# Optimization experiments

Measured on AMD Instinct MI355X. Metric: run time of the kernel, lower is better.

Reference implementation:

```python
import jax, jax.numpy as jnp
import numpy as np

B, S, D = 2, 2048, 1024
H = 16
HD = D // H  # 64
EPS = 1e-6
ROPE_BASE = 10000.0


def _rms_norm(x, w, eps=EPS):
    # torch nn.RMSNorm over last dim
    var = jnp.mean(jnp.square(x), axis=-1, keepdims=True)
    return x * jax.lax.rsqrt(var + eps) * w


def _rope_tables(seq_len, head_dim, base=ROPE_BASE):
    inv_freq = 1.0 / (base ** (jnp.arange(0, head_dim, 2, dtype=jnp.float32) / head_dim))
    t = jnp.arange(seq_len, dtype=jnp.float32)
    freqs = t[:, None] * inv_freq[None, :]            # [S, HD/2]
    emb = jnp.concatenate([freqs, freqs], axis=-1)    # [S, HD]
    return jnp.cos(emb), jnp.sin(emb)


def _rotate_half(x):
    x1, x2 = jnp.split(x, 2, axis=-1)
    return jnp.concatenate([-x2, x1], axis=-1)


def _apply_rope(x, cos, sin):
    # x: [B, H, S, HD]; cos/sin: [S, HD]
    return x * cos[None, None] + _rotate_half(x) * sin[None, None]


def setup_inputs() -> dict:
    key = jax.random.key(0)
    ks = jax.random.split(key, 8)
    scale = 1.0 / np.sqrt(D)
    return {
        "x": jax.random.normal(ks[0], (B, S, D), dtype=jnp.float32),
        "wq": jax.random.normal(ks[1], (D, D), dtype=jnp.float32) * scale,
        "wk": jax.random.normal(ks[2], (D, D), dtype=jnp.float32) * scale,
        "wv": jax.random.normal(ks[3], (D, D), dtype=jnp.float32) * scale,
        "wo": jax.random.normal(ks[4], (D, D), dtype=jnp.float32) * scale,
        "q_norm_w": jnp.ones((HD,), dtype=jnp.float32),
        "k_norm_w": jnp.ones((HD,), dtype=jnp.float32),
        "sink_logit": jnp.zeros((H,), dtype=jnp.float32),
    }


def reference(x, wq, wk, wv, wo, q_norm_w, k_norm_w, sink_logit):
    b, s, _ = x.shape
    # QKV projections (nn.Linear, no bias): y = x @ W^T
    q = jnp.einsum("bsd,od->bso", x, wq).reshape(b, s, H, HD)
    k = jnp.einsum("bsd,od->bso", x, wk).reshape(b, s, H, HD)
    v = jnp.einsum("bsd,od->bso", x, wv).reshape(b, s, H, HD)
    # QK RMSNorm (per head_dim)
    q = _rms_norm(q, q_norm_w)
    k = _rms_norm(k, k_norm_w)
    # [B, H, S, HD]
    q = q.transpose(0, 2, 1, 3)
    k = k.transpose(0, 2, 1, 3)
    v = v.transpose(0, 2, 1, 3)
    # full-head RoPE
    cos, sin = _rope_tables(s, HD)
    q = _apply_rope(q, cos, sin)
    k = _apply_rope(k, cos, sin)
    # manual attention with causal mask and sink softmax
    scale = HD ** -0.5
    scores = jnp.einsum("bhqd,bhkd->bhqk", q, k) * scale  # [B,H,S,S]
    causal = jnp.tril(jnp.ones((s, s), dtype=bool))
    scores = jnp.where(causal[None, None], scores, -jnp.inf)
    # sink-augmented softmax in fp32: append per-head sink logit, softmax, drop sink column
    sink = jnp.broadcast_to(sink_logit.astype(jnp.float32)[None, :, None, None], (b, H, s, 1))
    aug = jnp.concatenate([scores.astype(jnp.float32), sink], axis=-1)
    weights = jax.nn.softmax(aug, axis=-1)[..., :s].astype(scores.dtype)
    out = jnp.einsum("bhqk,bhkd->bhqd", weights, v)
    out = out.transpose(0, 2, 1, 3).reshape(b, s, D)
    return jnp.einsum("bsd,od->bso", out, wo)
```

## Files before the change

### kernel.cpp

```cpp
#include <hip/hip_runtime.h>

#define Bb 2
#define Ss 2048
#define Dd 1024
#define Hh 16
#define HDd 64
#define BS (Bb * Ss)

typedef __attribute__((ext_vector_type(8))) __bf16 bf16x8;
typedef __attribute__((ext_vector_type(8))) unsigned short u16x8;
typedef __attribute__((ext_vector_type(4))) float f32x4;

__device__ __forceinline__ unsigned short f2bf(float f) {
  union { float f; unsigned u; } v; v.f = f;
  unsigned r = v.u + 0x7fffu + ((v.u >> 16) & 1u);
  return (unsigned short)(r >> 16);
}
__device__ __forceinline__ unsigned short f2bf_fast(float f) {
  union { float f; unsigned u; } v; v.f = f;
  return (unsigned short)((v.u + 0x8000u) >> 16);
}

__device__ __forceinline__ void gl_lds16(const void* g, void* l) {
  __builtin_amdgcn_global_load_lds(
      (const __attribute__((address_space(1))) void*)g,
      (__attribute__((address_space(3))) void*)l, 16, 0, 0);
}

__global__ __launch_bounds__(256) void cast_all(
    const float4* __restrict__ x, const float4* __restrict__ wq,
    const float4* __restrict__ wk, const float4* __restrict__ wv,
    const float4* __restrict__ wo, ushort4* __restrict__ xb,
    ushort4* __restrict__ wqkvb, ushort4* __restrict__ wob,
    float* __restrict__ ct, float* __restrict__ st) {
  int i = blockIdx.x * 256 + threadIdx.x;
  const int NX4 = BS * Dd / 4;
  const int NW4 = Dd * Dd / 4;
  const float4* src;
  ushort4* dst;
  int idx;
  if (i < NX4) { src = x; dst = xb; idx = i; }
  else if ((i -= NX4) < NW4) { src = wq; dst = wqkvb; idx = i; }
  else if ((i -= NW4) < NW4) { src = wk; dst = wqkvb + NW4; idx = i; }
  else if ((i -= NW4) < NW4) { src = wv; dst = wqkvb + 2 * NW4; idx = i; }
  else if ((i -= NW4) < NW4) { src = wo; dst = wob; idx = i; }
  else if ((i -= NW4) < Ss * 32) {
    int s = i >> 5, jj = i & 31;
    float freq = __powf(10000.0f, -(float)jj * (1.0f / 32.0f));
    float cs, sn;
    sincosf((float)s * freq, &sn, &cs);
    ct[i] = cs; st[i] = sn;
    return;
  } else return;
  float4 v = src[idx];
  ushort4 o;
  o.x = f2bf(v.x); o.y = f2bf(v.y); o.z = f2bf(v.z); o.w = f2bf(v.w);
  dst[idx] = o;
}

__global__ __launch_bounds__(256, 3) void gemm_qkv(
    const unsigned short* __restrict__ A, const unsigned short* __restrict__ Bw,
    const float* __restrict__ qw, const float* __restrict__ kw,
    const float* __restrict__ ct, const float* __restrict__ st,
    unsigned short* __restrict__ Qb, unsigned short* __restrict__ Kb,
    unsigned short* __restrict__ Vt) {
  __shared__ __align__(16) unsigned short As[128 * 32];
  __shared__ __align__(16) unsigned short Bs[128 * 32];
  const int K = Dd, tid = threadIdx.x;
  const int lane = tid & 63;
  const int quad = lane >> 4;
  const int l16 = lane & 15;
  const int wave = tid >> 6;
  const int wm = (wave >> 1) * 64;
  const int wn = (wave & 1) * 64;
  const int tile_m = blockIdx.y * 128;
  const int tile_n = blockIdx.x * 128;

  const int off0 = tid * 16;
  const int off1 = 4096 + tid * 16;
  const int r0 = tid >> 2, r1 = r0 + 64;
  const int sch = (((tid & 3) ^ ((tid >> 3) & 3)) << 3);
  const int xg = ((quad ^ ((l16 >> 1) & 3)) << 3);

  const unsigned short* Ag0 = A + (size_t)(tile_m + r0) * K + sch;
  const unsigned short* Ag1 = A + (size_t)(tile_m + r1) * K + sch;
  const unsigned short* Bg0 = Bw + (size_t)(tile_n + r0) * K + sch;
  const unsigned short* Bg1 = Bw + (size_t)(tile_n + r1) * K + sch;

  f32x4 zero = {0.f, 0.f, 0.f, 0.f};
  f32x4 acc[4][4];
#pragma unroll
  for (int mi = 0; mi < 4; ++mi)
#pragma unroll
    for (int ni = 0; ni < 4; ++ni) acc[mi][ni] = zero;

  for (int k0 = 0; k0 < K; k0 += 32) {
    gl_lds16(Ag0 + k0, (char*)As + off0);
    gl_lds16(Ag1 + k0, (char*)As + off1);
    gl_lds16(Bg0 + k0, (char*)Bs + off0);
    gl_lds16(Bg1 + k0, (char*)Bs + off1);
    __syncthreads();
    bf16x8 af[4], bfv[4];
#pragma unroll
    for (int mi = 0; mi < 4; ++mi)
      af[mi] = *(const bf16x8*)&As[(wm + mi * 16 + l16) * 32 + xg];
#pragma unroll
    for (int ni = 0; ni < 4; ++ni)
      bfv[ni] = *(const bf16x8*)&Bs[(wn + ni * 16 + l16) * 32 + xg];
#pragma unroll
    for (int mi = 0; mi < 4; ++mi)
#pragma unroll
      for (int ni = 0; ni < 4; ++ni)
        acc[mi][ni] = __builtin_amdgcn_mfma_f32_16x16x32_bf16(
            af[mi], bfv[ni], acc[mi][ni], 0, 0, 0);
    __syncthreads();
  }

  const int type = blockIdx.x >> 3;
  const int h = (((blockIdx.x & 7) << 7) + wn) >> 6;
  const int bb = tile_m >> 11;
  const size_t bh = (size_t)bb * Hh + h;

  if (type == 2) {
#pragma unroll
    for (int mi = 0; mi < 4; ++mi) {
      int s0 = (tile_m + wm + mi * 16 + quad * 4) & (Ss - 1);
#pragma unroll
      for (int ni = 0; ni < 4; ++ni) {
        int d = ni * 16 + l16;
        ushort4 pv;
        pv.x = f2bf(acc[mi][ni][0]);
        pv.y = f2bf(acc[mi][ni][1]);
        pv.z = f2bf(acc[mi][ni][2]);
        pv.w = f2bf(acc[mi][ni][3]);
        *(ushort4*)&Vt[(bh * HDd + d) * Ss + s0] = pv;
      }
    }
  } else {
    const float* wnp = type ? kw : qw;
    unsigned short* Ob = type ? Kb : Qb;
    const float fscale = type ? 1.0f : 0.125f * 1.44269504f;
    float w0[4];
#pragma unroll
    for (int ni = 0; ni < 4; ++ni) w0[ni] = wnp[ni * 16 + l16];
#pragma unroll
    for (int mi = 0; mi < 4; ++mi) {
#pragma unroll
      for (int r = 0; r < 4; ++r) {
        int s = (tile_m + wm + mi * 16 + quad * 4 + r) & (Ss - 1);
        float ss2 = 0.f;
#pragma unroll
        for (int ni = 0; ni < 4; ++ni) ss2 += acc[mi][ni][r] * acc[mi][ni][r];
        ss2 += __shfl_xor(ss2, 1, 64);
        ss2 += __shfl_xor(ss2, 2, 64);
        ss2 += __shfl_xor(ss2, 4, 64);
        ss2 += __shfl_xor(ss2, 8, 64);
        float rr = rsqrtf(ss2 * (1.0f / 64.0f) + 1e-6f) * fscale;
        float c0 = ct[s * 32 + l16], c1 = ct[s * 32 + 16 + l16];
        float sn0 = st[s * 32 + l16], sn1 = st[s * 32 + 16 + l16];
#pragma unroll
        for (int ni = 0; ni < 4; ++ni) {
          float vn = acc[mi][ni][r] * rr * w0[ni];
          float vp = acc[mi][ni ^ 2][r] * rr * w0[ni ^ 2];
          float cs_ = (ni & 1) ? c1 : c0;
          float sn_ = (ni & 1) ? sn1 : sn0;
          float sg = (ni < 2) ? -1.0f : 1.0f;
          Ob[(bh * Ss + s) * HDd + ni * 16 + l16] = f2bf(vn * cs_ + sg * vp * sn_);
        }
      }
    }
  }
}

__global__ __launch_bounds__(256) void gemm_bt2(
    const unsigned short* __restrict__ A, const unsigned short* __restrict__ Bw,
    float* __restrict__ C, int M, int N, int K) {
  __shared__ __align__(16) unsigned short As[128 * 32];
  __shared__ __align__(16) unsigned short Bs[64 * 32];
  const int tid = threadIdx.x;
  const int lane = tid & 63;
  const int quad = lane >> 4;
  const int l16 = lane & 15;
  const int wave = tid >> 6;
  const int wm = (wave >> 1) * 64;
  const int wn = (wave & 1) * 32;
  const int tile_m = blockIdx.y * 128;
  const int tile_n = blockIdx.x * 64;

  const int off0 = tid * 16;
  const int off1 = 4096 + tid * 16;
  const int r0 = tid >> 2, r1 = r0 + 64;
  const int sch = (((tid & 3) ^ ((tid >> 3) & 3)) << 3);
  const int xg = ((quad ^ ((l16 >> 1) & 3)) << 3);

  const unsigned short* Ag0 = A + (size_t)(tile_m + r0) * K + sch;
  const unsigned short* Ag1 = A + (size_t)(tile_m + r1) * K + sch;
  const unsigned short* Bg0 = Bw + (size_t)(tile_n + r0) * K + sch;

  f32x4 zero = {0.f, 0.f, 0.f, 0.f};
  f32x4 acc[4][2];
#pragma unroll
  for (int mi = 0; mi < 4; ++mi)
#pragma unroll
    for (int ni = 0; ni < 2; ++ni) acc[mi][ni] = zero;

  for (int k0 = 0; k0 < K; k0 += 32) {
    gl_lds16(Ag0 + k0, (char*)As + off0);
    gl_lds16(Ag1 + k0, (char*)As + off1);
    gl_lds16(Bg0 + k0, (char*)Bs + off0);
    __syncthreads();
    bf16x8 af[4], bfv[2];
#pragma unroll
    for (int mi = 0; mi < 4; ++mi)
      af[mi] = *(const bf16x8*)&As[(wm + mi * 16 + l16) * 32 + xg];
#pragma unroll
    for (int ni = 0; ni < 2; ++ni)
      bfv[ni] = *(const bf16x8*)&Bs[(wn + ni * 16 + l16) * 32 + xg];
#pragma unroll
    for (int mi = 0; mi < 4; ++mi)
#pragma unroll
      for (int ni = 0; ni < 2; ++ni)
        acc[mi][ni] = __builtin_amdgcn_mfma_f32_16x16x32_bf16(
            af[mi], bfv[ni], acc[mi][ni], 0, 0, 0);
    __syncthreads();
  }

#pragma unroll
  for (int mi = 0; mi < 4; ++mi) {
#pragma unroll
    for (int ni = 0; ni < 2; ++ni) {
      int col = tile_n + wn + ni * 16 + l16;
#pragma unroll
      for (int r = 0; r < 4; ++r) {
        int row = tile_m + wm + mi * 16 + quad * 4 + r;
        C[(size_t)row * N + col] = acc[mi][ni][r];
      }
    }
  }
}

__global__ __launch_bounds__(256) void flash(
    const unsigned short* __restrict__ Qb, const unsigned short* __restrict__ Kb,
    const unsigned short* __restrict__ Vt, const float* __restrict__ sink,
    unsigned short* __restrict__ Ob) {
  __shared__ __align__(16) unsigned short Qs[64 * 64];
  __shared__ __align__(16) unsigned short Ks[2][64 * 64];
  __shared__ __align__(16) unsigned short Vs[3][64 * 64];
  __shared__ __align__(16) unsigned short Ps[4][16 * 72];

  int tid = threadIdx.x, lane = tid & 63, wave = tid >> 6;
  int quad = lane >> 4, l16 = lane & 15;
  int bx = blockIdx.x;
  int h = blockIdx.y, b = blockIdx.z;

  const unsigned short* Qg = Qb + ((size_t)(b * Hh + h) * Ss) * HDd;
  const unsigned short* Kg = Kb + ((size_t)(b * Hh + h) * Ss) * HDd;
  const unsigned short* Vg = Vt + ((size_t)(b * Hh + h) * HDd) * Ss;

  int off0 = tid * 16, off1 = 4096 + tid * 16;
  int sr0 = tid >> 3, sr1 = sr0 + 32;
  int sch = ((tid & 7) ^ (sr0 & 7)) * 8;
  int x0 = ((quad ^ (l16 & 7)) * 8);
  int x1 = x0 ^ 32;

  float sk = sink[h];
  f32x4 zero = {0.f, 0.f, 0.f, 0.f};

  bf16x8 ones;
  {
    u16x8 t;
#pragma unroll
    for (int i = 0; i < 8; ++i) t[i] = 0x3F80;
    ones = *(bf16x8*)&t;
  }

#pragma unroll 1
  for (int pass = 0; pass < 2; ++pass) {
    int qt = pass ? bx : 31 - bx;
    int q0 = qt * 64;
    int myq = q0 + wave * 16 + l16;

    __syncthreads();
    gl_lds16(Qg + (size_t)(q0 + sr0) * 64 + sch, (char*)Qs + off0);
    gl_lds16(Qg + (size_t)(q0 + sr1) * 64 + sch, (char*)Qs + off1);
    gl_lds16(Kg + (size_t)sr0 * 64 + sch, (char*)Ks[0] + off0);
    gl_lds16(Kg + (size_t)sr1 * 64 + sch, (char*)Ks[0] + off1);
    gl_lds16(Vg + (size_t)sr0 * Ss + sch, (char*)Vs[0] + off0);
    gl_lds16(Vg + (size_t)sr1 * Ss + sch, (char*)Vs[0] + off1);

    f32x4 Oacc[4], lacc = zero;
#pragma unroll
    for (int ni = 0; ni < 4; ++ni) Oacc[ni] = zero;

    __syncthreads();
    bf16x8 aq0 = *(const bf16x8*)&Qs[(wave * 16 + l16) * 64 + x0];
    bf16x8 aq1 = *(const bf16x8*)&Qs[(wave * 16 + l16) * 64 + x1];
    if (qt >= 1) {
      gl_lds16(Kg + (size_t)(64 + sr0) * 64 + sch, (char*)Ks[1] + off0);
      gl_lds16(Kg + (size_t)(64 + sr1) * 64 + sch, (char*)Ks[1] + off1);
      gl_lds16(Vg + (size_t)sr0 * Ss + 64 + sch, (char*)Vs[1] + off0);
      gl_lds16(Vg + (size_t)sr1 * Ss + 64 + sch, (char*)Vs[1] + off1);
    }

    f32x4 sc[4];
#pragma unroll
    for (int ni = 0; ni < 4; ++ni) {
      bf16x8 bk0 = *(const bf16x8*)&Ks[0][(ni * 16 + l16) * 64 + x0];
      bf16x8 bk1 = *(const bf16x8*)&Ks[0][(ni * 16 + l16) * 64 + x1];
      sc[ni] = __builtin_amdgcn_mfma_f32_16x16x32_bf16(bk0, aq0, zero, 0, 0, 0);
      sc[ni] = __builtin_amdgcn_mfma_f32_16x16x32_bf16(bk1, aq1, sc[ni], 0, 0, 0);
    }
    if (qt == 0) {
#pragma unroll
      for (int ni = 0; ni < 4; ++ni)
#pragma unroll
        for (int r = 0; r < 4; ++r)
          if (ni * 16 + quad * 4 + r > myq - q0) sc[ni][r] = -1.0e38f;
    }

    for (int kt = 0; kt <= qt; ++kt) {
      bool last = (kt == qt);
      if (!last) __syncthreads();
      if (kt + 2 <= qt) {
        int vb = (kt + 2) % 3, kb = kt & 1;
        gl_lds16(Kg + (size_t)((kt + 2) * 64 + sr0) * 64 + sch, (char*)Ks[kb] + off0);
        gl_lds16(Kg + (size_t)((kt + 2) * 64 + sr1) * 64 + sch, (char*)Ks[kb] + off1);
        gl_lds16(Vg + (size_t)sr0 * Ss + (kt + 2) * 64 + sch, (char*)Vs[vb] + off0);
        gl_lds16(Vg + (size_t)sr1 * Ss + (kt + 2) * 64 + sch, (char*)Vs[vb] + off1);
      }

#pragma unroll
      for (int ni = 0; ni < 4; ++ni) {
        ushort4 pk;
        pk.x = f2bf_fast(exp2f(sc[ni][0]));
        pk.y = f2bf_fast(exp2f(sc[ni][1]));
        pk.z = f2bf_fast(exp2f(sc[ni][2]));
        pk.w = f2bf_fast(exp2f(sc[ni][3]));
        *(ushort4*)&Ps[wave][l16 * 72 + ni * 16 + quad * 4] = pk;
      }

      f32x4 scn[4];
      if (!last) {
        const unsigned short* Kt = Ks[(kt + 1) & 1];
#pragma unroll
        for (int ni = 0; ni < 4; ++ni) {
          bf16x8 bk0 = *(const bf16x8*)&Kt[(ni * 16 + l16) * 64 + x0];
          bf16x8 bk1 = *(const bf16x8*)&Kt[(ni * 16 + l16) * 64 + x1];
          scn[ni] = __builtin_amdgcn_mfma_f32_16x16x32_bf16(bk0, aq0, zero, 0, 0, 0);
          scn[ni] = __builtin_amdgcn_mfma_f32_16x16x32_bf16(bk1, aq1, scn[ni], 0, 0, 0);
        }
        if (kt + 1 == qt) {
#pragma unroll
          for (int ni = 0; ni < 4; ++ni)
#pragma unroll
            for (int r = 0; r < 4; ++r)
              if ((kt + 1) * 64 + ni * 16 + quad * 4 + r > myq) scn[ni][r] = -1.0e38f;
        }
      }

      asm volatile("s_waitcnt lgkmcnt(0)" ::: "memory");
      bf16x8 ap0 = *(const bf16x8*)&Ps[wave][l16 * 72 + quad * 8];
      bf16x8 ap1 = *(const bf16x8*)&Ps[wave][l16 * 72 + 32 + quad * 8];

      const unsigned short* Vtile = Vs[kt % 3];
#pragma unroll
      for (int ni = 0; ni < 4; ++ni) {
        bf16x8 bv0 = *(const bf16x8*)&Vtile[(ni * 16 + l16) * 64 + x0];
        bf16x8 bv1 = *(const bf16x8*)&Vtile[(ni * 16 + l16) * 64 + x1];
        Oacc[ni] = __builtin_amdgcn_mfma_f32_16x16x32_bf16(bv0, ap0, Oacc[ni], 0, 0, 0);
        Oacc[ni] = __builtin_amdgcn_mfma_f32_16x16x32_bf16(bv1, ap1, Oacc[ni], 0, 0, 0);
      }
      lacc = __builtin_amdgcn_mfma_f32_16x16x32_bf16(ones, ap0, lacc, 0, 0, 0);
      lacc = __builtin_amdgcn_mfma_f32_16x16x32_bf16(ones, ap1, lacc, 0, 0, 0);

      if (!last) {
#pragma unroll
        for (int ni = 0; ni < 4; ++ni) sc[ni] = scn[ni];
      }
    }

    float inv = 1.0f / (lacc[0] + exp2f(sk * 1.44269504f));
#pragma unroll
    for (int ni = 0; ni < 4; ++ni) {
      ushort4 ov;
      ov.x = f2bf(Oacc[ni][0] * inv);
      ov.y = f2bf(Oacc[ni][1] * inv);
      ov.z = f2bf(Oacc[ni][2] * inv);
      ov.w = f2bf(Oacc[ni][3] * inv);
      *(ushort4*)&Ob[((size_t)b * Ss + myq) * Dd + h * 64 + ni * 16 + quad * 4] = ov;
    }
  }
}

extern "C" void kernel_launch(void* const* d_in, const int* in_sizes, int n_in,
                              void* d_out, int out_size, void* d_ws, size_t ws_size,
                              hipStream_t stream) {
  const float* x  = (const float*)d_in[0];
  const float* wq = (const float*)d_in[1];
  const float* wk = (const float*)d_in[2];
  const float* wv = (const float*)d_in[3];
  const float* wo = (const float*)d_in[4];
  const float* qw = (const float*)d_in[5];
  const float* kw = (const float*)d_in[6];
  const float* sk = (const float*)d_in[7];

  char* ws = (char*)d_ws;
  const size_t MB = 1ull << 20;
  unsigned short* xb    = (unsigned short*)(ws + 0);
  unsigned short* attnb = (unsigned short*)(ws + 0);
  unsigned short* wqkvb = (unsigned short*)(ws + 8 * MB);
  unsigned short* wob   = (unsigned short*)(ws + 14 * MB);
  float*          ct    = (float*)(ws + 16 * MB);
  float*          st    = (float*)(ws + 17 * MB);
  unsigned short* Qb    = (unsigned short*)(ws + 40 * MB);
  unsigned short* Kb    = (unsigned short*)(ws + 48 * MB);
  unsigned short* Vt    = (unsigned short*)(ws + 56 * MB);

  cast_all<<<8448, 256, 0, stream>>>(
      (const float4*)x, (const float4*)wq, (const float4*)wk, (const float4*)wv,
      (const float4*)wo, (ushort4*)xb, (ushort4*)wqkvb, (ushort4*)wob, ct, st);
  gemm_qkv<<<dim3(24, 32), 256, 0, stream>>>(xb, wqkvb, qw, kw, ct, st, Qb, Kb, Vt);
  flash<<<dim3(16, Hh, Bb), 256, 0, stream>>>(Qb, Kb, Vt, sk, attnb);
  gemm_bt2<<<dim3(16, 32), 256, 0, stream>>>(attnb, wob, (float*)d_out, BS, Dd, Dd);
}
```

Measured before the change: 189.6 us.

## Split flash attention into one q-tile per block with balanced 1D scheduling

The flash kernel now launches 1024 blocks, each handling a single query tile, instead of 512 blocks that each processed a paired long and short tile. A 1D block index is mapped so that short and long causal tiles interleave across launch order, and launch bounds request 4 blocks per CU. Q is loaded straight from global into registers instead of staging through LDS, the V buffer drops from triple to double buffering, and the P buffer uses an XOR swizzle instead of padding, all of which shrink LDS use. The aim is better occupancy and load balance, at the cost of less prefetch depth for V and possible register pressure under the tighter bound.

```diff
diff --git a/kernel.cpp b/kernel.cpp
--- a/kernel.cpp
+++ b/kernel.cpp
@@ -239,19 +239,22 @@
   }
 }
 
-__global__ __launch_bounds__(256) void flash(
+__global__ __launch_bounds__(256, 4) void flash(
     const unsigned short* __restrict__ Qb, const unsigned short* __restrict__ Kb,
     const unsigned short* __restrict__ Vt, const float* __restrict__ sink,
     unsigned short* __restrict__ Ob) {
-  __shared__ __align__(16) unsigned short Qs[64 * 64];
   __shared__ __align__(16) unsigned short Ks[2][64 * 64];
-  __shared__ __align__(16) unsigned short Vs[3][64 * 64];
-  __shared__ __align__(16) unsigned short Ps[4][16 * 72];
+  __shared__ __align__(16) unsigned short Vs[2][64 * 64];
+  __shared__ __align__(16) unsigned short Ps[4][16 * 64];
 
   int tid = threadIdx.x, lane = tid & 63, wave = tid >> 6;
   int quad = lane >> 4, l16 = lane & 15;
-  int bx = blockIdx.x;
-  int h = blockIdx.y, b = blockIdx.z;
+
+  int lid = blockIdx.x;
+  int g = lid >> 8, j = lid & 255;
+  int hb = j >> 3, t = j & 7;
+  int b = hb >> 4, h = hb & 15;
+  int qt = (g == 0) ? t : (g == 1) ? 31 - t : (g == 2) ? 8 + t : 23 - t;
 
   const unsigned short* Qg = Qb + ((size_t)(b * Hh + h) * Ss) * HDd;
   const unsigned short* Kg = Kb + ((size_t)(b * Hh + h) * Ss) * HDd;
@@ -263,132 +266,131 @@
   int x0 = ((quad ^ (l16 & 7)) * 8);
   int x1 = x0 ^ 32;
 
+  int q0 = qt * 64;
+  int myq = q0 + wave * 16 + l16;
+
   float sk = sink[h];
   f32x4 zero = {0.f, 0.f, 0.f, 0.f};
 
   bf16x8 ones;
   {
-    u16x8 t;
-#pragma unroll
-    for (int i = 0; i < 8; ++i) t[i] = 0x3F80;
-    ones = *(bf16x8*)&t;
-  }
-
-#pragma unroll 1
-  for (int pass = 0; pass < 2; ++pass) {
-    int qt = pass ? bx : 31 - bx;
-    int q0 = qt * 64;
-    int myq = q0 + wave * 16 + l16;
-
-    __syncthreads();
-    gl_lds16(Qg + (size_t)(q0 + sr0) * 64 + sch, (char*)Qs + off0);
-    gl_lds16(Qg + (size_t)(q0 + sr1) * 64 + sch, (char*)Qs + off1);
-    gl_lds16(Kg + (size_t)sr0 * 64 + sch, (char*)Ks[0] + off0);
-    gl_lds16(Kg + (size_t)sr1 * 64 + sch, (char*)Ks[0] + off1);
-    gl_lds16(Vg + (size_t)sr0 * Ss + sch, (char*)Vs[0] + off0);
-    gl_lds16(Vg + (size_t)sr1 * Ss + sch, (char*)Vs[0] + off1);
-
-    f32x4 Oacc[4], lacc = zero;
-#pragma unroll
-    for (int ni = 0; ni < 4; ++ni) Oacc[ni] = zero;
-
-    __syncthreads();
-    bf16x8 aq0 = *(const bf16x8*)&Qs[(wave * 16 + l16) * 64 + x0];
-    bf16x8 aq1 = *(const bf16x8*)&Qs[(wave * 16 + l16) * 64 + x1];
-    if (qt >= 1) {
-      gl_lds16(Kg + (size_t)(64 + sr0) * 64 + sch, (char*)Ks[1] + off0);
-      gl_lds16(Kg + (size_t)(64 + sr1) * 64 + sch, (char*)Ks[1] + off1);
-      gl_lds16(Vg + (size_t)sr0 * Ss + 64 + sch, (char*)Vs[1] + off0);
-      gl_lds16(Vg + (size_t)sr1 * Ss + 64 + sch, (char*)Vs[1] + off1);
-    }
-
-    f32x4 sc[4];
+    u16x8 tt;
+#pragma unroll
+    for (int i = 0; i < 8; ++i) tt[i] = 0x3F80;
+    ones = *(bf16x8*)&tt;
+  }
+
+  const unsigned short* Qrow = Qg + (size_t)myq * HDd;
+  bf16x8 aq0 = *(const bf16x8*)(Qrow + quad * 8);
+  bf16x8 aq1 = *(const bf16x8*)(Qrow + 32 + quad * 8);
+
+  gl_lds16(Kg + (size_t)sr0 * 64 + sch, (char*)Ks[0] + off0);
+  gl_lds16(Kg + (size_t)sr1 * 64 + sch, (char*)Ks[0] + off1);
+  gl_lds16(Vg + (size_t)sr0 * Ss + sch, (char*)Vs[0] + off0);
+  gl_lds16(Vg + (size_t)sr1 * Ss + sch, (char*)Vs[0] + off1);
+
+  f32x4 Oacc[4], lacc = zero;
+#pragma unroll
+  for (int ni = 0; ni < 4; ++ni) Oacc[ni] = zero;
+
+  __syncthreads();
+  if (qt >= 1) {
+    gl_lds16(Kg + (size_t)(64 + sr0) * 64 + sch, (char*)Ks[1] + off0);
+    gl_lds16(Kg + (size_t)(64 + sr1) * 64 + sch, (char*)Ks[1] + off1);
+  }
+
+  f32x4 sc[4];
+#pragma unroll
+  for (int ni = 0; ni < 4; ++ni) {
+    bf16x8 bk0 = *(const bf16x8*)&Ks[0][(ni * 16 + l16) * 64 + x0];
+    bf16x8 bk1 = *(const bf16x8*)&Ks[0][(ni * 16 + l16) * 64 + x1];
+    sc[ni] = __builtin_amdgcn_mfma_f32_16x16x32_bf16(bk0, aq0, zero, 0, 0, 0);
+    sc[ni] = __builtin_amdgcn_mfma_f32_16x16x32_bf16(bk1, aq1, sc[ni], 0, 0, 0);
+  }
+  if (qt == 0) {
+#pragma unroll
+    for (int ni = 0; ni < 4; ++ni)
+#pragma unroll
+      for (int r = 0; r < 4; ++r)
+        if (ni * 16 + quad * 4 + r > myq - q0) sc[ni][r] = -1.0e38f;
+  }
+
+  char* Pw = (char*)Ps[wave];
+  const int prow = l16 * 128;
+  const int psw = l16 & 7;
+
+  for (int kt = 0; kt <= qt; ++kt) {
+    bool last = (kt == qt);
+    if (qt > 0) __syncthreads();
+    if (kt + 2 <= qt) {
+      gl_lds16(Kg + (size_t)((kt + 2) * 64 + sr0) * 64 + sch, (char*)Ks[kt & 1] + off0);
+      gl_lds16(Kg + (size_t)((kt + 2) * 64 + sr1) * 64 + sch, (char*)Ks[kt & 1] + off1);
+    }
+    if (kt + 1 <= qt) {
+      gl_lds16(Vg + (size_t)sr0 * Ss + (kt + 1) * 64 + sch, (char*)Vs[(kt + 1) & 1] + off0);
+      gl_lds16(Vg + (size_t)sr1 * Ss + (kt + 1) * 64 + sch, (char*)Vs[(kt + 1) & 1] + off1);
+    }
+
 #pragma unroll
     for (int ni = 0; ni < 4; ++ni) {
-      bf16x8 bk0 = *(const bf16x8*)&Ks[0][(ni * 16 + l16) * 64 + x0];
-      bf16x8 bk1 = *(const bf16x8*)&Ks[0][(ni * 16 + l16) * 64 + x1];
-      sc[ni] = __builtin_amdgcn_mfma_f32_16x16x32_bf16(bk0, aq0, zero, 0, 0, 0);
-      sc[ni] = __builtin_amdgcn_mfma_f32_16x16x32_bf16(bk1, aq1, sc[ni], 0, 0, 0);
-    }
-    if (qt == 0) {
-#pragma unroll
-      for (int ni = 0; ni < 4; ++ni)
-#pragma unroll
-        for (int r = 0; r < 4; ++r)
-          if (ni * 16 + quad * 4 + r > myq - q0) sc[ni][r] = -1.0e38f;
-    }
-
-    for (int kt = 0; kt <= qt; ++kt) {
-      bool last = (kt == qt);
-      if (!last) __syncthreads();
-      if (kt + 2 <= qt) {
-        int vb = (kt + 2) % 3, kb = kt & 1;
-        gl_lds16(Kg + (size_t)((kt + 2) * 64 + sr0) * 64 + sch, (char*)Ks[kb] + off0);
-        gl_lds16(Kg + (size_t)((kt + 2) * 64 + sr1) * 64 + sch, (char*)Ks[kb] + off1);
-        gl_lds16(Vg + (size_t)sr0 * Ss + (kt + 2) * 64 + sch, (char*)Vs[vb] + off0);
-        gl_lds16(Vg + (size_t)sr1 * Ss + (kt + 2) * 64 + sch, (char*)Vs[vb] + off1);
+      ushort4 pk;
+      pk.x = f2bf_fast(exp2f(sc[ni][0]));
+      pk.y = f2bf_fast(exp2f(sc[ni][1]));
+      pk.z = f2bf_fast(exp2f(sc[ni][2]));
+      pk.w = f2bf_fast(exp2f(sc[ni][3]));
+      int chunk = (ni * 2 + (quad >> 1)) ^ psw;
+      *(ushort4*)(Pw + prow + chunk * 16 + (quad & 1) * 8) = pk;
+    }
+
+    f32x4 scn[4];
+    if (!last) {
+      const unsigned short* Kt = Ks[(kt + 1) & 1];
+#pragma unroll
+      for (int ni = 0; ni < 4; ++ni) {
+        bf16x8 bk0 = *(const bf16x8*)&Kt[(ni * 16 + l16) * 64 + x0];
+        bf16x8 bk1 = *(const bf16x8*)&Kt[(ni * 16 + l16) * 64 + x1];
+        scn[ni] = __builtin_amdgcn_mfma_f32_16x16x32_bf16(bk0, aq0, zero, 0, 0, 0);
+        scn[ni] = __builtin_amdgcn_mfma_f32_16x16x32_bf16(bk1, aq1, scn[ni], 0, 0, 0);
       }
-
-#pragma unroll
-      for (int ni = 0; ni < 4; ++ni) {
-        ushort4 pk;
-        pk.x = f2bf_fast(exp2f(sc[ni][0]));
-        pk.y = f2bf_fast(exp2f(sc[ni][1]));
-        pk.z = f2bf_fast(exp2f(sc[ni][2]));
-        pk.w = f2bf_fast(exp2f(sc[ni][3]));
-        *(ushort4*)&Ps[wave][l16 * 72 + ni * 16 + quad * 4] = pk;
+      if (kt + 1 == qt) {
+#pragma unroll
+        for (int ni = 0; ni < 4; ++ni)
+#pragma unroll
+          for (int r = 0; r < 4; ++r)
+            if ((kt + 1) * 64 + ni * 16 + quad * 4 + r > myq) scn[ni][r] = -1.0e38f;
       }
-
-      f32x4 scn[4];
-      if (!last) {
-        const unsigned short* Kt = Ks[(kt + 1) & 1];
-#pragma unroll
-        for (int ni = 0; ni < 4; ++ni) {
-          bf16x8 bk0 = *(const bf16x8*)&Kt[(ni * 16 + l16) * 64 + x0];
-          bf16x8 bk1 = *(const bf16x8*)&Kt[(ni * 16 + l16) * 64 + x1];
-          scn[ni] = __builtin_amdgcn_mfma_f32_16x16x32_bf16(bk0, aq0, zero, 0, 0, 0);
-          scn[ni] = __builtin_amdgcn_mfma_f32_16x16x32_bf16(bk1, aq1, scn[ni], 0, 0, 0);
-        }
-        if (kt + 1 == qt) {
-#pragma unroll
-          for (int ni = 0; ni < 4; ++ni)
-#pragma unroll
-            for (int r = 0; r < 4; ++r)
-              if ((kt + 1) * 64 + ni * 16 + quad * 4 + r > myq) scn[ni][r] = -1.0e38f;
-        }
-      }
-
-      asm volatile("s_waitcnt lgkmcnt(0)" ::: "memory");
-      bf16x8 ap0 = *(const bf16x8*)&Ps[wave][l16 * 72 + quad * 8];
-      bf16x8 ap1 = *(const bf16x8*)&Ps[wave][l16 * 72 + 32 + quad * 8];
-
-      const unsigned short* Vtile = Vs[kt % 3];
-#pragma unroll
-      for (int ni = 0; ni < 4; ++ni) {
-        bf16x8 bv0 = *(const bf16x8*)&Vtile[(ni * 16 + l16) * 64 + x0];
-        bf16x8 bv1 = *(const bf16x8*)&Vtile[(ni * 16 + l16) * 64 + x1];
-        Oacc[ni] = __builtin_amdgcn_mfma_f32_16x16x32_bf16(bv0, ap0, Oacc[ni], 0, 0, 0);
-        Oacc[ni] = __builtin_amdgcn_mfma_f32_16x16x32_bf16(bv1, ap1, Oacc[ni], 0, 0, 0);
-      }
-      lacc = __builtin_amdgcn_mfma_f32_16x16x32_bf16(ones, ap0, lacc, 0, 0, 0);
-      lacc = __builtin_amdgcn_mfma_f32_16x16x32_bf16(ones, ap1, lacc, 0, 0, 0);
-
-      if (!last) {
-#pragma unroll
-        for (int ni = 0; ni < 4; ++ni) sc[ni] = scn[ni];
-      }
-    }
-
-    float inv = 1.0f / (lacc[0] + exp2f(sk * 1.44269504f));
+    }
+
+    asm volatile("s_waitcnt lgkmcnt(0)" ::: "memory");
+    bf16x8 ap0 = *(const bf16x8*)(Pw + prow + ((quad ^ psw) * 16));
+    bf16x8 ap1 = *(const bf16x8*)(Pw + prow + (((quad + 4) ^ psw) * 16));
+
+    const unsigned short* Vtile = Vs[kt & 1];
 #pragma unroll
     for (int ni = 0; ni < 4; ++ni) {
-      ushort4 ov;
-      ov.x = f2bf(Oacc[ni][0] * inv);
-      ov.y = f2bf(Oacc[ni][1] * inv);
-      ov.z = f2bf(Oacc[ni][2] * inv);
-      ov.w = f2bf(Oacc[ni][3] * inv);
-      *(ushort4*)&Ob[((size_t)b * Ss + myq) * Dd + h * 64 + ni * 16 + quad * 4] = ov;
-    }
+      bf16x8 bv0 = *(const bf16x8*)&Vtile[(ni * 16 + l16) * 64 + x0];
+      bf16x8 bv1 = *(const bf16x8*)&Vtile[(ni * 16 + l16) * 64 + x1];
+      Oacc[ni] = __builtin_amdgcn_mfma_f32_16x16x32_bf16(bv0, ap0, Oacc[ni], 0, 0, 0);
+      Oacc[ni] = __builtin_amdgcn_mfma_f32_16x16x32_bf16(bv1, ap1, Oacc[ni], 0, 0, 0);
+    }
+    lacc = __builtin_amdgcn_mfma_f32_16x16x32_bf16(ones, ap0, lacc, 0, 0, 0);
+    lacc = __builtin_amdgcn_mfma_f32_16x16x32_bf16(ones, ap1, lacc, 0, 0, 0);
+
+    if (!last) {
+#pragma unroll
+      for (int ni = 0; ni < 4; ++ni) sc[ni] = scn[ni];
+    }
+  }
+
+  float inv = 1.0f / (lacc[0] + exp2f(sk * 1.44269504f));
+#pragma unroll
+  for (int ni = 0; ni < 4; ++ni) {
+    ushort4 ov;
+    ov.x = f2bf(Oacc[ni][0] * inv);
+    ov.y = f2bf(Oacc[ni][1] * inv);
+    ov.z = f2bf(Oacc[ni][2] * inv);
+    ov.w = f2bf(Oacc[ni][3] * inv);
+    *(ushort4*)&Ob[((size_t)b * Ss + myq) * Dd + h * 64 + ni * 16 + quad * 4] = ov;
   }
 }
 
@@ -420,6 +422,6 @@
       (const float4*)x, (const float4*)wq, (const float4*)wk, (const float4*)wv,
       (const float4*)wo, (ushort4*)xb, (ushort4*)wqkvb, (ushort4*)wob, ct, st);
   gemm_qkv<<<dim3(24, 32), 256, 0, stream>>>(xb, wqkvb, qw, kw, ct, st, Qb, Kb, Vt);
-  flash<<<dim3(16, Hh, Bb), 256, 0, stream>>>(Qb, Kb, Vt, sk, attnb);
+  flash<<<dim3(1024), 256, 0, stream>>>(Qb, Kb, Vt, sk, attnb);
   gemm_bt2<<<dim3(16, 32), 256, 0, stream>>>(attnb, wob, (float*)d_out, BS, Dd, Dd);
 }
```

Result: faster. 182.7 us (-3.7%).
